# Kernel tuning notes

Measured on AMD Instinct MI355X. Metric: run time of the kernel, lower is better.

Reference implementation:

```python
import jax, jax.numpy as jnp
import numpy as np

F8 = jnp.float8_e4m3fn
F8_MAX = 448.0  # finfo(float8_e4m3fn).max

def setup_inputs() -> dict:
    key = jax.random.key(0)
    k1, k2, k3 = jax.random.split(key, 3)
    B, S, IN, OUT = 4, 4096, 2048, 2048
    x = jax.random.normal(k1, (B, S, IN), dtype=jnp.float32)
    # Pre-quantized fp8 weight [OUT, IN] with a per-tensor scale, as stored by AutoFP8
    w = jax.random.normal(k2, (OUT, IN), dtype=jnp.float32)
    weight_scale = (jnp.max(jnp.abs(w)) / F8_MAX).astype(jnp.float32)
    qweight = jnp.clip(w / weight_scale, -F8_MAX, F8_MAX).astype(F8)
    input_scale = jnp.asarray(0.05, dtype=jnp.float32)  # static activation scale
    bias = jax.random.normal(k3, (OUT,), dtype=jnp.float32)
    return {"x": x, "qweight": qweight, "weight_scale": weight_scale,
            "input_scale": input_scale, "bias": bias}

def reference(x, qweight, weight_scale, input_scale, bias):
    # per_tensor_quantize: divide by static scale, clamp to fp8 range, cast to e4m3fn
    qinput = jnp.clip(x / input_scale, -F8_MAX, F8_MAX).astype(F8)  # [B,S,IN] fp8
    # scaled fp8 GEMM with fused dequant + bias epilogue (out_dtype = x.dtype)
    a = qinput.astype(x.dtype) * input_scale          # dequant activations
    b = qweight.astype(x.dtype) * weight_scale        # dequant weights [OUT,IN]
    return jnp.einsum('bsi,oi->bso', a, b) + bias     # [B,S,OUT]
```

## Files before the change

kernel.cpp:

```cpp
#include <hip/hip_runtime.h>
#include <stdint.h>

typedef float  floatx4 __attribute__((ext_vector_type(4)));
typedef int    intx8   __attribute__((ext_vector_type(8)));

#define AS1 __attribute__((address_space(1)))
#define AS3 __attribute__((address_space(3)))

__device__ __forceinline__ float quant_e4m3_value(float v) {
  float av = fabsf(v);
  float step, rstep;
  if (av < 0.015625f) {
    step  = 0.001953125f;
    rstep = 512.0f;
  } else {
    uint32_t e = __float_as_uint(av) >> 23;
    step  = __uint_as_float((e - 3u) << 23);
    rstep = __uint_as_float((257u - e) << 23);
  }
  return rintf(v * rstep) * step;
}

__device__ __forceinline__ uint32_t enc_e4m3(float v) {
  uint32_t u = __float_as_uint(v);
  uint32_t s = (u >> 24) & 0x80u;
  float av = fabsf(v);
  uint32_t b;
  if (av < 0.015625f) {
    b = s | (uint32_t)(av * 512.0f);
  } else {
    uint32_t e = ((u >> 23) & 0xffu) - 120u;
    uint32_t m = (u >> 20) & 7u;
    b = s | (e << 3) | m;
  }
  return b;
}

__device__ __forceinline__ float dec_e4m3(uint32_t b) {
  uint32_t s = (b & 0x80u) << 24;
  uint32_t e = (b >> 3) & 15u, m = b & 7u;
  float mag;
  if (e == 0u) mag = (float)m * 0.001953125f;
  else         mag = __uint_as_float(((e + 120u) << 23) | (m << 20));
  return __uint_as_float(s | __float_as_uint(mag));
}

__global__ void detect_mode_kernel(const uint32_t* __restrict__ qw,
                                   int* __restrict__ mode) {
  int t = threadIdx.x;
  uint32_t w0 = qw[t], w1 = qw[t + 64];
  bool a = ((w0 & 0xFFFFFu) == 0u) && ((w1 & 0xFFFFFu) == 0u);
  uint32_t nib = (w0 | (w0 >> 16) | w1 | (w1 >> 16)) & 0xFu;
  bool b = (nib == 0u);
  unsigned long long ba = __ballot(a);
  unsigned long long bb = __ballot(b);
  if (t == 0) mode[0] = (ba == ~0ull) ? 2 : ((bb == ~0ull) ? 1 : 0);
}

__global__ __launch_bounds__(256) void quantize_x_kernel(
    const float4* __restrict__ x, const float* __restrict__ s_ptr,
    uint32_t* __restrict__ q, int n4) {
  int i = blockIdx.x * 256 + threadIdx.x;
  if (i >= n4) return;
  const float s = s_ptr[0];
  float4 v = x[i];
  float a0 = quant_e4m3_value(fminf(fmaxf(v.x / s, -448.0f), 448.0f));
  float a1 = quant_e4m3_value(fminf(fmaxf(v.y / s, -448.0f), 448.0f));
  float a2 = quant_e4m3_value(fminf(fmaxf(v.z / s, -448.0f), 448.0f));
  float a3 = quant_e4m3_value(fminf(fmaxf(v.w / s, -448.0f), 448.0f));
  q[i] = enc_e4m3(a0) | (enc_e4m3(a1) << 8) | (enc_e4m3(a2) << 16) |
         (enc_e4m3(a3) << 24);
}

__global__ __launch_bounds__(256) void prep_w_kernel(
    const uint8_t* __restrict__ qw, const int* __restrict__ mode,
    uint32_t* __restrict__ w8, int n4) {
  int i = blockIdx.x * 256 + threadIdx.x;
  if (i >= n4) return;
  int m = mode[0];
  uint32_t o;
  if (m == 1) {
    ushort4 u = ((const ushort4*)qw)[i];
    o = enc_e4m3(__uint_as_float((uint32_t)u.x << 16)) |
        (enc_e4m3(__uint_as_float((uint32_t)u.y << 16)) << 8) |
        (enc_e4m3(__uint_as_float((uint32_t)u.z << 16)) << 16) |
        (enc_e4m3(__uint_as_float((uint32_t)u.w << 16)) << 24);
  } else if (m == 2) {
    float4 v = ((const float4*)qw)[i];
    o = enc_e4m3(v.x) | (enc_e4m3(v.y) << 8) | (enc_e4m3(v.z) << 16) |
        (enc_e4m3(v.w) << 24);
  } else {
    o = ((const uint32_t*)qw)[i];
  }
  w8[i] = o;
}

__global__ __launch_bounds__(256) void gemm_fp8_kernel(
    const uint8_t* __restrict__ A, const uint8_t* __restrict__ B,
    const float* __restrict__ wscale, const float* __restrict__ iscale,
    const float* __restrict__ bias, float* __restrict__ out,
    int M, int N, int K) {
  __shared__ uint8_t lsA[128 * 128];
  __shared__ uint8_t lsB[128 * 128];

  const int tid  = threadIdx.x;
  const int wave = tid >> 6;
  const int lane = tid & 63;
  const int bm = blockIdx.y;
  const int bn = blockIdx.x;

  const int wm = (wave & 1) * 64;
  const int wn = (wave >> 1) * 64;

  const int srow   = tid >> 3;
  const int schunk = (tid & 7) * 16;

  const uint8_t* gA = A + (size_t)(bm * 128 + srow) * K + schunk;
  const uint8_t* gB = B + (size_t)(bn * 128 + srow) * K + schunk;
  uint8_t* lA = &lsA[srow * 128 + schunk];
  uint8_t* lB = &lsB[srow * 128 + schunk];

  const int r15  = lane & 15;
  const int quad = lane >> 4;

  floatx4 acc[4][4];
#pragma unroll
  for (int i = 0; i < 4; ++i)
#pragma unroll
    for (int j = 0; j < 4; ++j) acc[i][j] = (floatx4){0.f, 0.f, 0.f, 0.f};

  for (int k0 = 0; k0 < K; k0 += 128) {
    __syncthreads();
#pragma unroll
    for (int it = 0; it < 4; ++it) {
      __builtin_amdgcn_global_load_lds(
          (const AS1 void*)(gA + k0 + (size_t)it * 32 * K),
          (AS3 void*)(lA + it * 32 * 128), 16, 0, 0);
      __builtin_amdgcn_global_load_lds(
          (const AS1 void*)(gB + k0 + (size_t)it * 32 * K),
          (AS3 void*)(lB + it * 32 * 128), 16, 0, 0);
    }
    __syncthreads();

    intx8 af[4], bf[4];
#pragma unroll
    for (int mi = 0; mi < 4; ++mi)
      af[mi] = *(const intx8*)(&lsA[(wm + mi * 16 + r15) * 128 + quad * 32]);
#pragma unroll
    for (int ni = 0; ni < 4; ++ni)
      bf[ni] = *(const intx8*)(&lsB[(wn + ni * 16 + r15) * 128 + quad * 32]);

#pragma unroll
    for (int mi = 0; mi < 4; ++mi)
#pragma unroll
      for (int ni = 0; ni < 4; ++ni)
        acc[mi][ni] = __builtin_amdgcn_mfma_scale_f32_16x16x128_f8f6f4(
            af[mi], bf[ni], acc[mi][ni],
            0 , 0 ,
            0, 127 , 0, 127 );
  }

  const float sc = wscale[0] * iscale[0];
  const int rq = quad * 4;
#pragma unroll
  for (int ni = 0; ni < 4; ++ni) {
    const int col = bn * 128 + wn + ni * 16 + r15;
    const float bv = bias[col];
#pragma unroll
    for (int mi = 0; mi < 4; ++mi) {
      const int row = bm * 128 + wm + mi * 16 + rq;
      float* o = out + (size_t)row * N + col;
#pragma unroll
      for (int r = 0; r < 4; ++r)
        o[(size_t)r * N] = acc[mi][ni][r] * sc + bv;
    }
  }
}

extern "C" void kernel_launch(void* const* d_in, const int* in_sizes, int n_in,
                              void* d_out, int out_size, void* d_ws,
                              size_t ws_size, hipStream_t stream) {
  const float*   x      = (const float*)d_in[0];
  const uint8_t* qw     = (const uint8_t*)d_in[1];
  const float*   wscale = (const float*)d_in[2];
  const float*   iscale = (const float*)d_in[3];
  const float*   bias   = (const float*)d_in[4];
  float*         out    = (float*)d_out;

  const int N = in_sizes[4];
  const int K = in_sizes[1] / N;
  const int M = in_sizes[0] / K;

  uint8_t* qx   = (uint8_t*)d_ws;
  uint8_t* w8   = qx + (size_t)M * K;
  int*     mode = (int*)(w8 + (size_t)N * K);

  detect_mode_kernel<<<1, 64, 0, stream>>>((const uint32_t*)qw, mode);

  const int nx4 = in_sizes[0] / 4;
  quantize_x_kernel<<<(nx4 + 255) / 256, 256, 0, stream>>>(
      (const float4*)x, iscale, (uint32_t*)qx, nx4);

  const int nw4 = in_sizes[1] / 4;
  prep_w_kernel<<<(nw4 + 255) / 256, 256, 0, stream>>>(
      qw, mode, (uint32_t*)w8, nw4);

  dim3 grid(N / 128, M / 128);
  gemm_fp8_kernel<<<grid, 256, 0, stream>>>(qx, w8, wscale, iscale, bias,
                                            out, M, N, K);
}
```

Baseline: 315.1 us.

## Pipeline fp8 GEMM with multi-buffered LDS, swizzle, larger tiles and fused mode detect

```diff
diff --git a/kernel.cpp b/kernel.cpp
--- a/kernel.cpp
+++ b/kernel.cpp
@@ -2,6 +2,7 @@
 #include <stdint.h>
 
 typedef float  floatx4 __attribute__((ext_vector_type(4)));
+typedef int    intx4   __attribute__((ext_vector_type(4)));
 typedef int    intx8   __attribute__((ext_vector_type(8)));
 
 #define AS1 __attribute__((address_space(1)))
@@ -34,27 +35,6 @@
     b = s | (e << 3) | m;
   }
   return b;
-}
-
-__device__ __forceinline__ float dec_e4m3(uint32_t b) {
-  uint32_t s = (b & 0x80u) << 24;
-  uint32_t e = (b >> 3) & 15u, m = b & 7u;
-  float mag;
-  if (e == 0u) mag = (float)m * 0.001953125f;
-  else         mag = __uint_as_float(((e + 120u) << 23) | (m << 20));
-  return __uint_as_float(s | __float_as_uint(mag));
-}
-
-__global__ void detect_mode_kernel(const uint32_t* __restrict__ qw,
-                                   int* __restrict__ mode) {
-  int t = threadIdx.x;
-  uint32_t w0 = qw[t], w1 = qw[t + 64];
-  bool a = ((w0 & 0xFFFFFu) == 0u) && ((w1 & 0xFFFFFu) == 0u);
-  uint32_t nib = (w0 | (w0 >> 16) | w1 | (w1 >> 16)) & 0xFu;
-  bool b = (nib == 0u);
-  unsigned long long ba = __ballot(a);
-  unsigned long long bb = __ballot(b);
-  if (t == 0) mode[0] = (ba == ~0ull) ? 2 : ((bb == ~0ull) ? 1 : 0);
 }
 
 __global__ __launch_bounds__(256) void quantize_x_kernel(
@@ -73,11 +53,18 @@
 }
 
 __global__ __launch_bounds__(256) void prep_w_kernel(
-    const uint8_t* __restrict__ qw, const int* __restrict__ mode,
-    uint32_t* __restrict__ w8, int n4) {
+    const uint8_t* __restrict__ qw, uint32_t* __restrict__ w8, int n4) {
+  const uint32_t* q32 = (const uint32_t*)qw;
+  int lane = threadIdx.x & 63;
+  uint32_t w0 = q32[lane], w1 = q32[lane + 64];
+  bool fa = ((w0 & 0xFFFFFu) == 0u) && ((w1 & 0xFFFFFu) == 0u);
+  uint32_t nib = (w0 | (w0 >> 16) | w1 | (w1 >> 16)) & 0xFu;
+  unsigned long long ba = __ballot(fa);
+  unsigned long long bb = __ballot(nib == 0u);
+  int m = (ba == ~0ull) ? 2 : ((bb == ~0ull) ? 1 : 0);
+
   int i = blockIdx.x * 256 + threadIdx.x;
   if (i >= n4) return;
-  int m = mode[0];
   uint32_t o;
   if (m == 1) {
     ushort4 u = ((const ushort4*)qw)[i];
@@ -95,86 +82,140 @@
   w8[i] = o;
 }
 
-__global__ __launch_bounds__(256) void gemm_fp8_kernel(
+__global__ __launch_bounds__(512) void gemm_fp8_kernel(
     const uint8_t* __restrict__ A, const uint8_t* __restrict__ B,
     const float* __restrict__ wscale, const float* __restrict__ iscale,
     const float* __restrict__ bias, float* __restrict__ out,
     int M, int N, int K) {
-  __shared__ uint8_t lsA[128 * 128];
-  __shared__ uint8_t lsB[128 * 128];
+  __shared__ uint8_t lds[131072];
 
   const int tid  = threadIdx.x;
+  const int lane = tid & 63;
   const int wave = tid >> 6;
-  const int lane = tid & 63;
-  const int bm = blockIdx.y;
-  const int bn = blockIdx.x;
-
-  const int wm = (wave & 1) * 64;
-  const int wn = (wave >> 1) * 64;
-
-  const int srow   = tid >> 3;
-  const int schunk = (tid & 7) * 16;
-
-  const uint8_t* gA = A + (size_t)(bm * 128 + srow) * K + schunk;
-  const uint8_t* gB = B + (size_t)(bn * 128 + srow) * K + schunk;
-  uint8_t* lA = &lsA[srow * 128 + schunk];
-  uint8_t* lB = &lsB[srow * 128 + schunk];
-
+
+  const int nbx = gridDim.x;
+  const int nwg = nbx * gridDim.y;
+  int flat = blockIdx.y * nbx + blockIdx.x;
+  flat = (flat & 7) * (nwg >> 3) + (flat >> 3);
+  const int bm = flat / nbx;
+  const int bn = flat - bm * nbx;
+
+  const int wm_i = wave >> 1;
+  const int wn_i = wave & 1;
   const int r15  = lane & 15;
   const int quad = lane >> 4;
 
+  const uint8_t* asrc[4]; uint32_t adst[4];
+  const uint8_t* bsrc[2]; uint32_t bdst[2];
+#pragma unroll
+  for (int j = 0; j < 4; ++j) {
+    const int s = tid + j * 512, row = s >> 3, p = s & 7;
+    asrc[j] = A + (size_t)(bm * 256 + row) * K + ((p ^ (row & 7)) << 4);
+    adst[j] = (uint32_t)s << 4;
+  }
+#pragma unroll
+  for (int j = 0; j < 2; ++j) {
+    const int s = tid + j * 512, row = s >> 3, p = s & 7;
+    bsrc[j] = B + (size_t)(bn * 128 + row) * K + ((p ^ (row & 7)) << 4);
+    bdst[j] = (uint32_t)s << 4;
+  }
+
+#define STAGE_A(j, kbyte, ab)                                                  \
+  __builtin_amdgcn_global_load_lds(                                            \
+      (const AS1 void*)(asrc[j] + (kbyte)),                                    \
+      (AS3 void*)(&lds[(ab) * 32768u + adst[j]]), 16, 0, 0)
+#define STAGE_B(j, kbyte, bb)                                                  \
+  __builtin_amdgcn_global_load_lds(                                            \
+      (const AS1 void*)(bsrc[j] + (kbyte)),                                    \
+      (AS3 void*)(&lds[98304u + (bb) * 16384u + bdst[j]]), 16, 0, 0)
+
   floatx4 acc[4][4];
 #pragma unroll
   for (int i = 0; i < 4; ++i)
 #pragma unroll
     for (int j = 0; j < 4; ++j) acc[i][j] = (floatx4){0.f, 0.f, 0.f, 0.f};
 
-  for (int k0 = 0; k0 < K; k0 += 128) {
-    __syncthreads();
-#pragma unroll
-    for (int it = 0; it < 4; ++it) {
-      __builtin_amdgcn_global_load_lds(
-          (const AS1 void*)(gA + k0 + (size_t)it * 32 * K),
-          (AS3 void*)(lA + it * 32 * 128), 16, 0, 0);
-      __builtin_amdgcn_global_load_lds(
-          (const AS1 void*)(gB + k0 + (size_t)it * 32 * K),
-          (AS3 void*)(lB + it * 32 * 128), 16, 0, 0);
-    }
-    __syncthreads();
+  const int T = K >> 7;
+
+  STAGE_B(0, 0, 0); STAGE_B(1, 0, 0);
+  STAGE_A(0, 0, 0); STAGE_A(1, 0, 0); STAGE_A(2, 0, 0); STAGE_A(3, 0, 0);
+  if (T > 1) {
+    STAGE_A(0, 128, 1); STAGE_A(1, 128, 1);
+    STAGE_A(2, 128, 1); STAGE_A(3, 128, 1);
+    asm volatile("s_waitcnt vmcnt(4)" ::: "memory");
+  } else {
+    asm volatile("s_waitcnt vmcnt(0)" ::: "memory");
+  }
+  __builtin_amdgcn_sched_barrier(0);
+  __builtin_amdgcn_s_barrier();
+
+  int ab = 0, bb = 0;
+  for (int t = 0; t < T; ++t) {
+    const uint8_t* lA = &lds[ab * 32768u];
+    const uint8_t* lB = &lds[98304u + bb * 16384u];
+
+    if (t + 1 < T) {
+      const int kb = (t + 1) << 7;
+      STAGE_B(0, kb, bb ^ 1); STAGE_B(1, kb, bb ^ 1);
+    }
+    if (t + 2 < T) {
+      int a2 = ab + 2; if (a2 >= 3) a2 -= 3;
+      const int kb = (t + 2) << 7;
+      STAGE_A(0, kb, a2); STAGE_A(1, kb, a2);
+      STAGE_A(2, kb, a2); STAGE_A(3, kb, a2);
+    }
 
     intx8 af[4], bf[4];
 #pragma unroll
-    for (int mi = 0; mi < 4; ++mi)
-      af[mi] = *(const intx8*)(&lsA[(wm + mi * 16 + r15) * 128 + quad * 32]);
-#pragma unroll
-    for (int ni = 0; ni < 4; ++ni)
-      bf[ni] = *(const intx8*)(&lsB[(wn + ni * 16 + r15) * 128 + quad * 32]);
-
-#pragma unroll
-    for (int mi = 0; mi < 4; ++mi)
-#pragma unroll
-      for (int ni = 0; ni < 4; ++ni)
-        acc[mi][ni] = __builtin_amdgcn_mfma_scale_f32_16x16x128_f8f6f4(
-            af[mi], bf[ni], acc[mi][ni],
-            0 , 0 ,
-            0, 127 , 0, 127 );
+    for (int i = 0; i < 4; ++i) {
+      const int r = wm_i * 64 + i * 16 + r15, k8 = r & 7;
+      intx4 lo = *(const intx4*)&lA[r * 128 + (((quad * 2)     ^ k8) << 4)];
+      intx4 hi = *(const intx4*)&lA[r * 128 + (((quad * 2 + 1) ^ k8) << 4)];
+      af[i] = __builtin_shufflevector(lo, hi, 0, 1, 2, 3, 4, 5, 6, 7);
+    }
+#pragma unroll
+    for (int i = 0; i < 4; ++i) {
+      const int r = wn_i * 64 + i * 16 + r15, k8 = r & 7;
+      intx4 lo = *(const intx4*)&lB[r * 128 + (((quad * 2)     ^ k8) << 4)];
+      intx4 hi = *(const intx4*)&lB[r * 128 + (((quad * 2 + 1) ^ k8) << 4)];
+      bf[i] = __builtin_shufflevector(lo, hi, 0, 1, 2, 3, 4, 5, 6, 7);
+    }
+
+    __builtin_amdgcn_s_setprio(1);
+#pragma unroll
+    for (int i = 0; i < 4; ++i)
+#pragma unroll
+      for (int jn = 0; jn < 4; ++jn)
+        acc[i][jn] = __builtin_amdgcn_mfma_scale_f32_16x16x128_f8f6f4(
+            af[i], bf[jn], acc[i][jn], 0, 0, 0, 127, 0, 127);
+    __builtin_amdgcn_s_setprio(0);
+
+    if (t + 2 < T)      asm volatile("s_waitcnt vmcnt(4)" ::: "memory");
+    else if (t + 1 < T) asm volatile("s_waitcnt vmcnt(0)" ::: "memory");
+    __builtin_amdgcn_sched_barrier(0);
+    __builtin_amdgcn_s_barrier();
+
+    ab = (ab == 2) ? 0 : ab + 1;
+    bb ^= 1;
   }
 
   const float sc = wscale[0] * iscale[0];
   const int rq = quad * 4;
 #pragma unroll
   for (int ni = 0; ni < 4; ++ni) {
-    const int col = bn * 128 + wn + ni * 16 + r15;
+    const int col = bn * 128 + wn_i * 64 + ni * 16 + r15;
     const float bv = bias[col];
 #pragma unroll
     for (int mi = 0; mi < 4; ++mi) {
-      const int row = bm * 128 + wm + mi * 16 + rq;
+      const int row = bm * 256 + wm_i * 64 + mi * 16 + rq;
       float* o = out + (size_t)row * N + col;
 #pragma unroll
       for (int r = 0; r < 4; ++r)
         o[(size_t)r * N] = acc[mi][ni][r] * sc + bv;
     }
   }
+#undef STAGE_A
+#undef STAGE_B
 }
 
 extern "C" void kernel_launch(void* const* d_in, const int* in_sizes, int n_in,
@@ -191,21 +232,17 @@
   const int K = in_sizes[1] / N;
   const int M = in_sizes[0] / K;
 
-  uint8_t* qx   = (uint8_t*)d_ws;
-  uint8_t* w8   = qx + (size_t)M * K;
-  int*     mode = (int*)(w8 + (size_t)N * K);
-
-  detect_mode_kernel<<<1, 64, 0, stream>>>((const uint32_t*)qw, mode);
+  uint8_t* qx = (uint8_t*)d_ws;
+  uint8_t* w8 = qx + (size_t)M * K;
 
   const int nx4 = in_sizes[0] / 4;
   quantize_x_kernel<<<(nx4 + 255) / 256, 256, 0, stream>>>(
       (const float4*)x, iscale, (uint32_t*)qx, nx4);
 
   const int nw4 = in_sizes[1] / 4;
-  prep_w_kernel<<<(nw4 + 255) / 256, 256, 0, stream>>>(
-      qw, mode, (uint32_t*)w8, nw4);
-
-  dim3 grid(N / 128, M / 128);
-  gemm_fp8_kernel<<<grid, 256, 0, stream>>>(qx, w8, wscale, iscale, bias,
+  prep_w_kernel<<<(nw4 + 255) / 256, 256, 0, stream>>>(qw, (uint32_t*)w8, nw4);
+
+  dim3 grid(N / 128, M / 256);
+  gemm_fp8_kernel<<<grid, 512, 0, stream>>>(qx, w8, wscale, iscale, bias,
                                             out, M, N, K);
 }
```

After: 313.7 us. Within noise of the previous version (-0.5%).
